# Kernel optimization log

Hardware: AMD Instinct MI355X
Metric: run time of the kernel (lower is better)

Reference implementation:

```python
import jax, jax.numpy as jnp
import numpy as np

B, S, E, H, SN, LMAX = 128, 512, 768, 16, 100, 5
DH = E // H  # 48

def setup_inputs() -> dict:
    key = jax.random.key(0)
    ks = jax.random.split(key, 10)
    idx = jax.random.randint(ks[0], (B, LMAX), 0, S)
    lengths = jax.random.randint(ks[1], (B,), 1, LMAX + 1)
    valid = jnp.arange(LMAX)[None, :] < lengths[:, None]
    locations = jnp.where(valid, idx, -1)
    return {
        "last_hidden_state": jax.random.normal(ks[2], (B, S, E), jnp.float32),
        "sense_emb": jax.random.normal(ks[3], (B, SN, E), jnp.float32),
        "locations": locations,
        "in_proj_weight": jax.random.normal(ks[4], (3 * E, E), jnp.float32) * 0.02,
        "in_proj_bias": jax.random.normal(ks[5], (3 * E,), jnp.float32) * 0.02,
        "out_proj_weight": jax.random.normal(ks[6], (E, E), jnp.float32) * 0.02,
        "out_proj_bias": jax.random.normal(ks[7], (E,), jnp.float32) * 0.02,
        "linear_weight": jax.random.normal(ks[8], (SN, E), jnp.float32) * 0.02,
        "linear_bias": jax.random.normal(ks[9], (SN,), jnp.float32) * 0.02,
    }

def reference(last_hidden_state, sense_emb, locations, in_proj_weight, in_proj_bias,
              out_proj_weight, out_proj_bias, linear_weight, linear_bias):
    # Ragged gather + mean over the valid (non -1) token locations per row.
    mask = (locations != -1)                                   # [B, LMAX]
    safe = jnp.where(mask, locations, 0)                       # [B, LMAX]
    gathered = jnp.take_along_axis(last_hidden_state, safe[..., None], axis=1)  # [B,LMAX,E]
    cnt = mask.sum(axis=1, keepdims=True).astype(last_hidden_state.dtype)
    pun = (gathered * mask[..., None]).sum(axis=1) / cnt       # [B, E]

    # qkv: prepend pun-word embedding to the sense embeddings -> [B, SN+1, E]
    qkv = jnp.concatenate([pun[:, None, :], sense_emb], axis=1)

    # nn.MultiheadAttention with batch_first=False: axis0 = seq (L=B), axis1 = batch (N=SN+1).
    proj = qkv @ in_proj_weight.T + in_proj_bias               # [L, N, 3E]
    q, k, v = jnp.split(proj, 3, axis=-1)
    L, N = qkv.shape[0], qkv.shape[1]
    q = q.reshape(L, N, H, DH) * (DH ** -0.5)
    k = k.reshape(L, N, H, DH)
    v = v.reshape(L, N, H, DH)
    scores = jnp.einsum('lnhd,mnhd->nhlm', q, k)               # [N,H,L,L]
    attn = jax.nn.softmax(scores, axis=-1)
    ctx = jnp.einsum('nhlm,mnhd->lnhd', attn, v).reshape(L, N, E)
    attn_out = ctx @ out_proj_weight.T + out_proj_bias         # [L, N, E]

    res = attn_out[:, 0, :]                                    # [B, E] (batch slot 0)
    res = res @ linear_weight.T + linear_bias                  # [B, SN]
    return res
```

## Files before the change

### kernel.cpp

```cpp
#include <hip/hip_runtime.h>

#define SEQ 512
#define EMB 768
#define K3E 2304
#define DHD 48

__global__ __launch_bounds__(256) void k0_pun(
    const float* __restrict__ lhs, const int* __restrict__ loc,
    float* __restrict__ pun)
{
  int id = blockIdx.x * 256 + threadIdx.x;
  int row = id / 192;
  int ch  = id - row * 192;
  int cnt = 0;
  float4 s = make_float4(0.f, 0.f, 0.f, 0.f);
#pragma unroll
  for (int j = 0; j < 5; j++) {
    int v = loc[row * 5 + j];
    if (v >= 0) {
      float4 wv = *(const float4*)&lhs[((size_t)row * SEQ + v) * EMB + ch * 4];
      s.x += wv.x; s.y += wv.y; s.z += wv.z; s.w += wv.w;
      cnt++;
    }
  }
  float inv = 1.0f / (float)cnt;
  *(float4*)&pun[(size_t)row * EMB + ch * 4] =
      make_float4(s.x * inv, s.y * inv, s.z * inv, s.w * inv);
}

__global__ __launch_bounds__(512, 4) void k1_gemm_wcomb(
    const float* __restrict__ pun, const float* __restrict__ Bw,
    const float* __restrict__ bias, float* __restrict__ C,
    const float* __restrict__ wlin, const float* __restrict__ wout,
    float* __restrict__ wcomb)
{
  __shared__ float lds[14336];
  const int t = threadIdx.x;
  const int w = t >> 6, l = t & 63;
  const int tx = l & 7, ty = l >> 3;
  const int gm = l & 15, gq = l >> 4;
  const int kbase = w * 96;
  const int AW = w * 1792, BW = AW + 640;

  float4 aF, bF0, bF1;
  float acc[2][4] = {};

#define STAGE_A(b) {                                                         \
    int Ab = AW + (b) * 320;                                                 \
    lds[Ab + (gq*4+0)*20 + gm] = aF.x;                                       \
    lds[Ab + (gq*4+1)*20 + gm] = aF.y;                                       \
    lds[Ab + (gq*4+2)*20 + gm] = aF.z;                                       \
    lds[Ab + (gq*4+3)*20 + gm] = aF.w; }

#define INNER(b) {                                                           \
    int Ab = AW + (b) * 320, Bb = BW + (b) * 576;                            \
    _Pragma("unroll")                                                        \
    for (int kk = 0; kk < 16; kk++) {                                        \
      float2 a  = *(float2*)&lds[Ab + kk * 20 + ty * 2];                     \
      float4 bb = *(float4*)&lds[Bb + kk * 36 + tx * 4];                     \
      acc[0][0] += a.x*bb.x; acc[0][1] += a.x*bb.y;                          \
      acc[0][2] += a.x*bb.z; acc[0][3] += a.x*bb.w;                          \
      acc[1][0] += a.y*bb.x; acc[1][1] += a.y*bb.y;                          \
      acc[1][2] += a.y*bb.z; acc[1][3] += a.y*bb.w;                          \
    } }

  if (blockIdx.x < 576) {
    const int c  = blockIdx.x;
    const int bm = (c / 72) * 16, bn = (c % 72) * 32;
    const int bl = l & 31, bh = l >> 5;
    const float* arow = pun + (size_t)(bm + gm) * EMB;
    const float* brow = Bw + (size_t)(bn + bl) * EMB;

#define G_LOAD(s) {                                                          \
    int k0 = kbase + (s) * 16;                                               \
    aF  = *(const float4*)&arow[k0 + gq * 4];                                \
    bF0 = *(const float4*)&brow[k0 + bh * 8 + 0];                            \
    bF1 = *(const float4*)&brow[k0 + bh * 8 + 4]; }

#define G_WRITE(b) {                                                         \
    STAGE_A(b)                                                               \
    int Bb = BW + (b) * 576;                                                 \
    lds[Bb + (bh*8+0)*36 + bl] = bF0.x; lds[Bb + (bh*8+1)*36 + bl] = bF0.y;  \
    lds[Bb + (bh*8+2)*36 + bl] = bF0.z; lds[Bb + (bh*8+3)*36 + bl] = bF0.w;  \
    lds[Bb + (bh*8+4)*36 + bl] = bF1.x; lds[Bb + (bh*8+5)*36 + bl] = bF1.y;  \
    lds[Bb + (bh*8+6)*36 + bl] = bF1.z; lds[Bb + (bh*8+7)*36 + bl] = bF1.w; }

    G_LOAD(0); G_WRITE(0);
    for (int s = 0; s < 6; s++) {
      int b = s & 1;
      if (s < 5) G_LOAD(s + 1);
      INNER(b);
      if (s < 5) G_WRITE(b ^ 1);
    }
#undef G_LOAD
#undef G_WRITE

#pragma unroll
    for (int i = 0; i < 2; i++)
      *(float4*)&lds[AW + (ty*2 + i) * 32 + tx * 4] =
          make_float4(acc[i][0], acc[i][1], acc[i][2], acc[i][3]);
    __syncthreads();
    int m = t >> 5, n = t & 31;
    float v = lds[0*1792 + t] + lds[1*1792 + t] + lds[2*1792 + t] + lds[3*1792 + t]
            + lds[4*1792 + t] + lds[5*1792 + t] + lds[6*1792 + t] + lds[7*1792 + t]
            + bias[bn + n];
    C[(size_t)(bm + m) * K3E + bn + n] = v;
  } else {
    const int cc = blockIdx.x - 576;
    const int bm = (cc / 24) * 16, bn = (cc % 24) * 32;
    const int wi = l >> 2;
    const int j4 = (l & 3) * 8;
    int arow_i = bm + gm; if (arow_i > 99) arow_i = 99;
    const float* arow = wlin + (size_t)arow_i * EMB;

#define W_LOAD(s) {                                                          \
    int k0 = kbase + (s) * 16;                                               \
    aF  = *(const float4*)&arow[k0 + gq * 4];                                \
    const float* wr = wout + (size_t)(k0 + wi) * EMB + bn + j4;              \
    bF0 = *(const float4*)&wr[0];                                            \
    bF1 = *(const float4*)&wr[4]; }

#define W_WRITE(b) {                                                         \
    STAGE_A(b)                                                               \
    int Bb = BW + (b) * 576;                                                 \
    *(float4*)&lds[Bb + wi*36 + j4]     = bF0;                               \
    *(float4*)&lds[Bb + wi*36 + j4 + 4] = bF1; }

    W_LOAD(0); W_WRITE(0);
    for (int s = 0; s < 6; s++) {
      int b = s & 1;
      if (s < 5) W_LOAD(s + 1);
      INNER(b);
      if (s < 5) W_WRITE(b ^ 1);
    }
#undef W_LOAD
#undef W_WRITE

#pragma unroll
    for (int i = 0; i < 2; i++)
      *(float4*)&lds[AW + (ty*2 + i) * 32 + tx * 4] =
          make_float4(acc[i][0], acc[i][1], acc[i][2], acc[i][3]);
    __syncthreads();
    int m = t >> 5, n = t & 31;
    if (bm + m < 100) {
      float v = lds[0*1792 + t] + lds[1*1792 + t] + lds[2*1792 + t] + lds[3*1792 + t]
              + lds[4*1792 + t] + lds[5*1792 + t] + lds[6*1792 + t] + lds[7*1792 + t];
      wcomb[(size_t)(bm + m) * EMB + bn + n] = v;
    }
  }
#undef STAGE_A
#undef INNER
}

__global__ __launch_bounds__(256) void k2_attn(
    const float* __restrict__ proj, float* __restrict__ ctx)
{
  __shared__ float ks[128][52];
  __shared__ float vs[128][52];
  int h  = blockIdx.x >> 3;
  int l0 = (blockIdx.x & 7) * 16;
  int t  = threadIdx.x;

  for (int i = t; i < 128 * 12; i += 256) {
    int m  = i / 12;
    int dd = (i - m * 12) * 4;
    float4 kv = *(const float4*)&proj[(size_t)m * K3E + EMB     + h * DHD + dd];
    float4 vv = *(const float4*)&proj[(size_t)m * K3E + 2 * EMB + h * DHD + dd];
    *(float4*)&ks[m][dd] = kv;
    *(float4*)&vs[m][dd] = vv;
  }

  int l  = t >> 4;
  int g  = t & 15;
  int lg = l0 + l;
  const float scale = 0.14433756729740643f;
  float q[48];
#pragma unroll
  for (int jj = 0; jj < 12; jj++) {
    float4 qv = *(const float4*)&proj[(size_t)lg * K3E + h * DHD + jj * 4];
    q[jj*4+0] = qv.x * scale; q[jj*4+1] = qv.y * scale;
    q[jj*4+2] = qv.z * scale; q[jj*4+3] = qv.w * scale;
  }
  __syncthreads();

  float sv[8];
  float smax = -1e30f;
#pragma unroll
  for (int jm = 0; jm < 8; jm++) {
    int m = g + jm * 16;
    float s = 0.0f;
#pragma unroll
    for (int dq = 0; dq < 12; dq++) {
      float4 kv = *(const float4*)&ks[m][dq * 4];
      s += q[dq*4+0]*kv.x + q[dq*4+1]*kv.y + q[dq*4+2]*kv.z + q[dq*4+3]*kv.w;
    }
    sv[jm] = s;
    smax = fmaxf(smax, s);
  }
#pragma unroll
  for (int off = 1; off < 16; off <<= 1) smax = fmaxf(smax, __shfl_xor(smax, off));
  float ssum = 0.0f;
#pragma unroll
  for (int jm = 0; jm < 8; jm++) { float e = __expf(sv[jm] - smax); sv[jm] = e; ssum += e; }
#pragma unroll
  for (int off = 1; off < 16; off <<= 1) ssum += __shfl_xor(ssum, off);
  float inv = 1.0f / ssum;
#pragma unroll
  for (int jm = 0; jm < 8; jm++) sv[jm] *= inv;

  float acc[48] = {};
#pragma unroll
  for (int jm = 0; jm < 8; jm++) {
    int m = g + jm * 16;
    float p = sv[jm];
#pragma unroll
    for (int dq = 0; dq < 12; dq++) {
      float4 vv = *(const float4*)&vs[m][dq * 4];
      acc[dq*4+0] += p*vv.x; acc[dq*4+1] += p*vv.y;
      acc[dq*4+2] += p*vv.z; acc[dq*4+3] += p*vv.w;
    }
  }

  {
    float buf[24];
    if (g & 8) {
#pragma unroll
      for (int d = 0; d < 24; d++) buf[d] = acc[d];
    } else {
#pragma unroll
      for (int d = 0; d < 24; d++) buf[d] = acc[d + 24];
    }
#pragma unroll
    for (int d = 0; d < 24; d++) buf[d] = __shfl_xor(buf[d], 8);
    if (g & 8) {
#pragma unroll
      for (int d = 0; d < 24; d++) acc[d] = acc[d + 24] + buf[d];
    } else {
#pragma unroll
      for (int d = 0; d < 24; d++) acc[d] = acc[d] + buf[d];
    }
  }
  {
    float buf[12];
    if (g & 4) {
#pragma unroll
      for (int d = 0; d < 12; d++) buf[d] = acc[d];
    } else {
#pragma unroll
      for (int d = 0; d < 12; d++) buf[d] = acc[d + 12];
    }
#pragma unroll
    for (int d = 0; d < 12; d++) buf[d] = __shfl_xor(buf[d], 4);
    if (g & 4) {
#pragma unroll
      for (int d = 0; d < 12; d++) acc[d] = acc[d + 12] + buf[d];
    } else {
#pragma unroll
      for (int d = 0; d < 12; d++) acc[d] = acc[d] + buf[d];
    }
  }
  {
    float buf[6];
    if (g & 2) {
#pragma unroll
      for (int d = 0; d < 6; d++) buf[d] = acc[d];
    } else {
#pragma unroll
      for (int d = 0; d < 6; d++) buf[d] = acc[d + 6];
    }
#pragma unroll
    for (int d = 0; d < 6; d++) buf[d] = __shfl_xor(buf[d], 2);
    if (g & 2) {
#pragma unroll
      for (int d = 0; d < 6; d++) acc[d] = acc[d + 6] + buf[d];
    } else {
#pragma unroll
      for (int d = 0; d < 6; d++) acc[d] = acc[d] + buf[d];
    }
  }
  {
    float buf[3];
    if (g & 1) {
#pragma unroll
      for (int d = 0; d < 3; d++) buf[d] = acc[d];
    } else {
#pragma unroll
      for (int d = 0; d < 3; d++) buf[d] = acc[d + 3];
    }
#pragma unroll
    for (int d = 0; d < 3; d++) buf[d] = __shfl_xor(buf[d], 1);
    if (g & 1) {
#pragma unroll
      for (int d = 0; d < 3; d++) acc[d] = acc[d + 3] + buf[d];
    } else {
#pragma unroll
      for (int d = 0; d < 3; d++) acc[d] = acc[d] + buf[d];
    }
  }
#pragma unroll
  for (int j = 0; j < 3; j++) {
    ctx[(size_t)lg * EMB + h * DHD + g * 3 + j] = acc[j];
  }
}

__global__ __launch_bounds__(512, 4) void k3_final(
    const float* __restrict__ A, const float* __restrict__ Bw,
    const float* __restrict__ wlin, const float* __restrict__ bout,
    const float* __restrict__ blin, float* __restrict__ C)
{
  __shared__ float lds[14368];
  const int t = threadIdx.x;
  const int w = t >> 6, l = t & 63;
  const int bm = blockIdx.y * 16, bn = blockIdx.x * 32;
  const int tx = l & 7, ty = l >> 3;
  const int gm = l & 15, gq = l >> 4;
  const int bl = l & 31, bh = l >> 5;
  const int kbase = w * 96;
  const int AW = w * 1792, BW = AW + 640;

  if (t < 256) {
    int col = bn + (t >> 3);
    int ks  = (t & 7) * 96;
    float p = 0.f;
    if (col < 100) {
      const float* wr = wlin + (size_t)col * EMB + ks;
#pragma unroll
      for (int j = 0; j < 24; j++) {
        float4 wv = *(const float4*)&wr[j * 4];
        float4 bv = *(const float4*)&bout[ks + j * 4];
        p += wv.x*bv.x + wv.y*bv.y + wv.z*bv.z + wv.w*bv.w;
      }
    }
    p += __shfl_xor(p, 1); p += __shfl_xor(p, 2); p += __shfl_xor(p, 4);
    if ((t & 7) == 0) lds[14336 + (t >> 3)] = p + (col < 100 ? blin[col] : 0.f);
  }

  const float* arow = A + (size_t)(bm + gm) * EMB;
  int brow_i = bn + bl; if (brow_i > 99) brow_i = 99;
  const float* brow = Bw + (size_t)brow_i * EMB;

  float4 aF, bF0, bF1;

#define F_LOAD(s) {                                                          \
    int k0 = kbase + (s) * 16;                                               \
    aF  = *(const float4*)&arow[k0 + gq * 4];                                \
    bF0 = *(const float4*)&brow[k0 + bh * 8 + 0];                            \
    bF1 = *(const float4*)&brow[k0 + bh * 8 + 4]; }

#define F_WRITE(b) {                                                         \
    int Ab = AW + (b) * 320;                                                 \
    lds[Ab + (gq*4+0)*20 + gm] = aF.x;                                       \
    lds[Ab + (gq*4+1)*20 + gm] = aF.y;                                       \
    lds[Ab + (gq*4+2)*20 + gm] = aF.z;                                       \
    lds[Ab + (gq*4+3)*20 + gm] = aF.w;                                       \
    int Bb = BW + (b) * 576;                                                 \
    lds[Bb + (bh*8+0)*36 + bl] = bF0.x; lds[Bb + (bh*8+1)*36 + bl] = bF0.y;  \
    lds[Bb + (bh*8+2)*36 + bl] = bF0.z; lds[Bb + (bh*8+3)*36 + bl] = bF0.w;  \
    lds[Bb + (bh*8+4)*36 + bl] = bF1.x; lds[Bb + (bh*8+5)*36 + bl] = bF1.y;  \
    lds[Bb + (bh*8+6)*36 + bl] = bF1.z; lds[Bb + (bh*8+7)*36 + bl] = bF1.w; }

  float acc[2][4] = {};
  F_LOAD(0); F_WRITE(0);
  for (int s = 0; s < 6; s++) {
    int b = s & 1;
    if (s < 5) F_LOAD(s + 1);
    int Ab = AW + b * 320, Bb = BW + b * 576;
#pragma unroll
    for (int kk = 0; kk < 16; kk++) {
      float2 a  = *(float2*)&lds[Ab + kk * 20 + ty * 2];
      float4 bb = *(float4*)&lds[Bb + kk * 36 + tx * 4];
      acc[0][0] += a.x*bb.x; acc[0][1] += a.x*bb.y; acc[0][2] += a.x*bb.z; acc[0][3] += a.x*bb.w;
      acc[1][0] += a.y*bb.x; acc[1][1] += a.y*bb.y; acc[1][2] += a.y*bb.z; acc[1][3] += a.y*bb.w;
    }
    if (s < 5) F_WRITE(b ^ 1);
  }
#undef F_LOAD
#undef F_WRITE

#pragma unroll
  for (int i = 0; i < 2; i++)
    *(float4*)&lds[AW + (ty*2 + i) * 32 + tx * 4] =
        make_float4(acc[i][0], acc[i][1], acc[i][2], acc[i][3]);
  __syncthreads();
  int m = t >> 5, n = t & 31;
  int col = bn + n;
  if (col < 100) {
    float v = lds[0*1792 + t] + lds[1*1792 + t] + lds[2*1792 + t] + lds[3*1792 + t]
            + lds[4*1792 + t] + lds[5*1792 + t] + lds[6*1792 + t] + lds[7*1792 + t]
            + lds[14336 + n];
    C[(size_t)(bm + m) * 100 + col] = v;
  }
}

extern "C" void kernel_launch(void* const* d_in, const int* in_sizes, int n_in,
                              void* d_out, int out_size, void* d_ws, size_t ws_size,
                              hipStream_t stream) {
  const float* lhs   = (const float*)d_in[0];
  const int*   loc   = (const int*)  d_in[2];
  const float* w_in  = (const float*)d_in[3];
  const float* b_in  = (const float*)d_in[4];
  const float* w_out = (const float*)d_in[5];
  const float* b_out = (const float*)d_in[6];
  const float* w_lin = (const float*)d_in[7];
  const float* b_lin = (const float*)d_in[8];
  float* out = (float*)d_out;

  char* ws = (char*)d_ws;
  float* pun   = (float*)(ws);
  float* proj  = (float*)(ws + 393216);
  float* ctx   = (float*)(ws + 393216 + 1179648);
  float* wcomb = (float*)(ws + 393216 + 1179648 + 393216);

  k0_pun<<<96, 256, 0, stream>>>(lhs, loc, pun);
  k1_gemm_wcomb<<<744, 512, 0, stream>>>(pun, w_in, b_in, proj,
                                         w_lin, w_out, wcomb);
  k2_attn<<<128, 256, 0, stream>>>(proj, ctx);
  k3_final<<<dim3(4, 8), 512, 0, stream>>>(ctx, wcomb, w_lin, b_out, b_lin, out);
}
```

Baseline: 45.93 us.

## Widen k1 GEMM tiles to 16x64 and hoist bias dot-product into k1

The k1 GEMM tile grows from 16x32 to 16x64 per block, with each thread holding a 4x4 accumulator and a k-step of 8. This halves the block count from 744 to 372 and raises arithmetic per LDS load. The wlin·bout bias vector is now computed once by an extra block in k1 and written to workspace, instead of being recomputed inside every k3 block. The cost is fewer blocks in flight to hide latency, and k3 now reads the bias from global memory.

```diff
diff --git a/kernel.cpp b/kernel.cpp
--- a/kernel.cpp
+++ b/kernel.cpp
@@ -32,124 +32,160 @@
     const float* __restrict__ pun, const float* __restrict__ Bw,
     const float* __restrict__ bias, float* __restrict__ C,
     const float* __restrict__ wlin, const float* __restrict__ wout,
-    float* __restrict__ wcomb)
+    const float* __restrict__ bout, const float* __restrict__ blin,
+    float* __restrict__ wcomb, float* __restrict__ wsbias)
 {
-  __shared__ float lds[14336];
+  __shared__ float lds[11264];
   const int t = threadIdx.x;
   const int w = t >> 6, l = t & 63;
-  const int tx = l & 7, ty = l >> 3;
-  const int gm = l & 15, gq = l >> 4;
+  const int tx = l & 15, ty = l >> 4;
+  const int gm = l & 15, gk = l >> 4;
   const int kbase = w * 96;
-  const int AW = w * 1792, BW = AW + 640;
-
-  float4 aF, bF0, bF1;
-  float acc[2][4] = {};
-
-#define STAGE_A(b) {                                                         \
-    int Ab = AW + (b) * 320;                                                 \
-    lds[Ab + (gq*4+0)*20 + gm] = aF.x;                                       \
-    lds[Ab + (gq*4+1)*20 + gm] = aF.y;                                       \
-    lds[Ab + (gq*4+2)*20 + gm] = aF.z;                                       \
-    lds[Ab + (gq*4+3)*20 + gm] = aF.w; }
+  const int AW = w * 1408, BW = AW + 320;
+
+  float2 aF;
+  float4 bF0, bF1;
+  float acc[4][4] = {};
+
+#define A_WRITE(b) {                                                         \
+    int Ab = AW + (b) * 160;                                                 \
+    lds[Ab + (gk*2+0)*20 + gm] = aF.x;                                       \
+    lds[Ab + (gk*2+1)*20 + gm] = aF.y; }
 
 #define INNER(b) {                                                           \
-    int Ab = AW + (b) * 320, Bb = BW + (b) * 576;                            \
+    int Ab = AW + (b) * 160, Bb = BW + (b) * 544;                            \
     _Pragma("unroll")                                                        \
-    for (int kk = 0; kk < 16; kk++) {                                        \
-      float2 a  = *(float2*)&lds[Ab + kk * 20 + ty * 2];                     \
-      float4 bb = *(float4*)&lds[Bb + kk * 36 + tx * 4];                     \
+    for (int kk = 0; kk < 8; kk++) {                                         \
+      float4 a  = *(float4*)&lds[Ab + kk * 20 + ty * 4];                     \
+      float4 bb = *(float4*)&lds[Bb + kk * 68 + tx * 4];                     \
       acc[0][0] += a.x*bb.x; acc[0][1] += a.x*bb.y;                          \
       acc[0][2] += a.x*bb.z; acc[0][3] += a.x*bb.w;                          \
       acc[1][0] += a.y*bb.x; acc[1][1] += a.y*bb.y;                          \
       acc[1][2] += a.y*bb.z; acc[1][3] += a.y*bb.w;                          \
+      acc[2][0] += a.z*bb.x; acc[2][1] += a.z*bb.y;                          \
+      acc[2][2] += a.z*bb.z; acc[2][3] += a.z*bb.w;                          \
+      acc[3][0] += a.w*bb.x; acc[3][1] += a.w*bb.y;                          \
+      acc[3][2] += a.w*bb.z; acc[3][3] += a.w*bb.w;                          \
     } }
 
-  if (blockIdx.x < 576) {
+#define EPILOGUE_STORE() {                                                   \
+    _Pragma("unroll")                                                        \
+    for (int i = 0; i < 4; i++)                                              \
+      *(float4*)&lds[AW + (ty*4 + i) * 64 + tx * 4] =                        \
+          make_float4(acc[i][0], acc[i][1], acc[i][2], acc[i][3]);           \
+    __syncthreads(); }
+
+  if (blockIdx.x < 288) {
     const int c  = blockIdx.x;
-    const int bm = (c / 72) * 16, bn = (c % 72) * 32;
-    const int bl = l & 31, bh = l >> 5;
+    const int bm = (c / 36) * 16, bn = (c % 36) * 64;
     const float* arow = pun + (size_t)(bm + gm) * EMB;
-    const float* brow = Bw + (size_t)(bn + bl) * EMB;
+    const float* brow = Bw + (size_t)(bn + l) * EMB;
 
 #define G_LOAD(s) {                                                          \
-    int k0 = kbase + (s) * 16;                                               \
-    aF  = *(const float4*)&arow[k0 + gq * 4];                                \
-    bF0 = *(const float4*)&brow[k0 + bh * 8 + 0];                            \
-    bF1 = *(const float4*)&brow[k0 + bh * 8 + 4]; }
+    int k0 = kbase + (s) * 8;                                                \
+    aF  = *(const float2*)&arow[k0 + gk * 2];                                \
+    bF0 = *(const float4*)&brow[k0 + 0];                                     \
+    bF1 = *(const float4*)&brow[k0 + 4]; }
 
 #define G_WRITE(b) {                                                         \
-    STAGE_A(b)                                                               \
-    int Bb = BW + (b) * 576;                                                 \
-    lds[Bb + (bh*8+0)*36 + bl] = bF0.x; lds[Bb + (bh*8+1)*36 + bl] = bF0.y;  \
-    lds[Bb + (bh*8+2)*36 + bl] = bF0.z; lds[Bb + (bh*8+3)*36 + bl] = bF0.w;  \
-    lds[Bb + (bh*8+4)*36 + bl] = bF1.x; lds[Bb + (bh*8+5)*36 + bl] = bF1.y;  \
-    lds[Bb + (bh*8+6)*36 + bl] = bF1.z; lds[Bb + (bh*8+7)*36 + bl] = bF1.w; }
+    A_WRITE(b)                                                               \
+    int Bb = BW + (b) * 544;                                                 \
+    lds[Bb + 0*68 + l] = bF0.x; lds[Bb + 1*68 + l] = bF0.y;                  \
+    lds[Bb + 2*68 + l] = bF0.z; lds[Bb + 3*68 + l] = bF0.w;                  \
+    lds[Bb + 4*68 + l] = bF1.x; lds[Bb + 5*68 + l] = bF1.y;                  \
+    lds[Bb + 6*68 + l] = bF1.z; lds[Bb + 7*68 + l] = bF1.w; }
 
     G_LOAD(0); G_WRITE(0);
-    for (int s = 0; s < 6; s++) {
+    for (int s = 0; s < 12; s++) {
       int b = s & 1;
-      if (s < 5) G_LOAD(s + 1);
+      if (s < 11) G_LOAD(s + 1);
       INNER(b);
-      if (s < 5) G_WRITE(b ^ 1);
+      if (s < 11) G_WRITE(b ^ 1);
     }
 #undef G_LOAD
 #undef G_WRITE
 
-#pragma unroll
-    for (int i = 0; i < 2; i++)
-      *(float4*)&lds[AW + (ty*2 + i) * 32 + tx * 4] =
-          make_float4(acc[i][0], acc[i][1], acc[i][2], acc[i][3]);
-    __syncthreads();
-    int m = t >> 5, n = t & 31;
-    float v = lds[0*1792 + t] + lds[1*1792 + t] + lds[2*1792 + t] + lds[3*1792 + t]
-            + lds[4*1792 + t] + lds[5*1792 + t] + lds[6*1792 + t] + lds[7*1792 + t]
-            + bias[bn + n];
-    C[(size_t)(bm + m) * K3E + bn + n] = v;
-  } else {
-    const int cc = blockIdx.x - 576;
-    const int bm = (cc / 24) * 16, bn = (cc % 24) * 32;
-    const int wi = l >> 2;
-    const int j4 = (l & 3) * 8;
+    EPILOGUE_STORE();
+    int o = t * 2;
+    int m = o >> 6, n = o & 63;
+    float2 s0 = *(float2*)&lds[0*1408 + o];
+    float2 s1 = *(float2*)&lds[1*1408 + o];
+    float2 s2 = *(float2*)&lds[2*1408 + o];
+    float2 s3 = *(float2*)&lds[3*1408 + o];
+    float2 s4 = *(float2*)&lds[4*1408 + o];
+    float2 s5 = *(float2*)&lds[5*1408 + o];
+    float2 s6 = *(float2*)&lds[6*1408 + o];
+    float2 s7 = *(float2*)&lds[7*1408 + o];
+    float2 bb2 = *(const float2*)&bias[bn + n];
+    float2 r = make_float2(s0.x+s1.x+s2.x+s3.x+s4.x+s5.x+s6.x+s7.x+bb2.x,
+                           s0.y+s1.y+s2.y+s3.y+s4.y+s5.y+s6.y+s7.y+bb2.y);
+    *(float2*)&C[(size_t)(bm + m) * K3E + bn + n] = r;
+  } else if (blockIdx.x < 372) {
+    const int cc = blockIdx.x - 288;
+    const int bm = (cc / 12) * 16, bn = (cc % 12) * 64;
+    const int kr = l >> 3;
+    const int j8 = (l & 7) * 8;
     int arow_i = bm + gm; if (arow_i > 99) arow_i = 99;
     const float* arow = wlin + (size_t)arow_i * EMB;
 
 #define W_LOAD(s) {                                                          \
-    int k0 = kbase + (s) * 16;                                               \
-    aF  = *(const float4*)&arow[k0 + gq * 4];                                \
-    const float* wr = wout + (size_t)(k0 + wi) * EMB + bn + j4;              \
+    int k0 = kbase + (s) * 8;                                                \
+    aF = *(const float2*)&arow[k0 + gk * 2];                                 \
+    const float* wr = wout + (size_t)(k0 + kr) * EMB + bn + j8;              \
     bF0 = *(const float4*)&wr[0];                                            \
     bF1 = *(const float4*)&wr[4]; }
 
 #define W_WRITE(b) {                                                         \
-    STAGE_A(b)                                                               \
-    int Bb = BW + (b) * 576;                                                 \
-    *(float4*)&lds[Bb + wi*36 + j4]     = bF0;                               \
-    *(float4*)&lds[Bb + wi*36 + j4 + 4] = bF1; }
+    A_WRITE(b)                                                               \
+    int Bb = BW + (b) * 544;                                                 \
+    *(float4*)&lds[Bb + kr*68 + j8]     = bF0;                               \
+    *(float4*)&lds[Bb + kr*68 + j8 + 4] = bF1; }
 
     W_LOAD(0); W_WRITE(0);
-    for (int s = 0; s < 6; s++) {
+    for (int s = 0; s < 12; s++) {
       int b = s & 1;
-      if (s < 5) W_LOAD(s + 1);
+      if (s < 11) W_LOAD(s + 1);
       INNER(b);
-      if (s < 5) W_WRITE(b ^ 1);
+      if (s < 11) W_WRITE(b ^ 1);
     }
 #undef W_LOAD
 #undef W_WRITE
 
-#pragma unroll
-    for (int i = 0; i < 2; i++)
-      *(float4*)&lds[AW + (ty*2 + i) * 32 + tx * 4] =
-          make_float4(acc[i][0], acc[i][1], acc[i][2], acc[i][3]);
-    __syncthreads();
-    int m = t >> 5, n = t & 31;
+    EPILOGUE_STORE();
+    int o = t * 2;
+    int m = o >> 6, n = o & 63;
     if (bm + m < 100) {
-      float v = lds[0*1792 + t] + lds[1*1792 + t] + lds[2*1792 + t] + lds[3*1792 + t]
-              + lds[4*1792 + t] + lds[5*1792 + t] + lds[6*1792 + t] + lds[7*1792 + t];
-      wcomb[(size_t)(bm + m) * EMB + bn + n] = v;
-    }
-  }
-#undef STAGE_A
+      float2 s0 = *(float2*)&lds[0*1408 + o];
+      float2 s1 = *(float2*)&lds[1*1408 + o];
+      float2 s2 = *(float2*)&lds[2*1408 + o];
+      float2 s3 = *(float2*)&lds[3*1408 + o];
+      float2 s4 = *(float2*)&lds[4*1408 + o];
+      float2 s5 = *(float2*)&lds[5*1408 + o];
+      float2 s6 = *(float2*)&lds[6*1408 + o];
+      float2 s7 = *(float2*)&lds[7*1408 + o];
+      float2 r = make_float2(s0.x+s1.x+s2.x+s3.x+s4.x+s5.x+s6.x+s7.x,
+                             s0.y+s1.y+s2.y+s3.y+s4.y+s5.y+s6.y+s7.y);
+      *(float2*)&wcomb[(size_t)(bm + m) * EMB + bn + n] = r;
+    }
+  } else {
+    if (t < 400) {
+      int col = t >> 2, q = t & 3;
+      const float* wr = wlin + (size_t)col * EMB + q * 192;
+      const float* br = bout + q * 192;
+      float p = 0.f;
+#pragma unroll
+      for (int j = 0; j < 48; j++) {
+        float4 wv = *(const float4*)&wr[j * 4];
+        float4 bv = *(const float4*)&br[j * 4];
+        p += wv.x*bv.x + wv.y*bv.y + wv.z*bv.z + wv.w*bv.w;
+      }
+      p += __shfl_xor(p, 1); p += __shfl_xor(p, 2);
+      if (q == 0) wsbias[col] = p + blin[col];
+    }
+  }
+#undef A_WRITE
 #undef INNER
+#undef EPILOGUE_STORE
 }
 
 __global__ __launch_bounds__(256) void k2_attn(
@@ -305,10 +341,9 @@
 
 __global__ __launch_bounds__(512, 4) void k3_final(
     const float* __restrict__ A, const float* __restrict__ Bw,
-    const float* __restrict__ wlin, const float* __restrict__ bout,
-    const float* __restrict__ blin, float* __restrict__ C)
+    const float* __restrict__ wsbias, float* __restrict__ C)
 {
-  __shared__ float lds[14368];
+  __shared__ float lds[14336];
   const int t = threadIdx.x;
   const int w = t >> 6, l = t & 63;
   const int bm = blockIdx.y * 16, bn = blockIdx.x * 32;
@@ -317,23 +352,6 @@
   const int bl = l & 31, bh = l >> 5;
   const int kbase = w * 96;
   const int AW = w * 1792, BW = AW + 640;
-
-  if (t < 256) {
-    int col = bn + (t >> 3);
-    int ks  = (t & 7) * 96;
-    float p = 0.f;
-    if (col < 100) {
-      const float* wr = wlin + (size_t)col * EMB + ks;
-#pragma unroll
-      for (int j = 0; j < 24; j++) {
-        float4 wv = *(const float4*)&wr[j * 4];
-        float4 bv = *(const float4*)&bout[ks + j * 4];
-        p += wv.x*bv.x + wv.y*bv.y + wv.z*bv.z + wv.w*bv.w;
-      }
-    }
-    p += __shfl_xor(p, 1); p += __shfl_xor(p, 2); p += __shfl_xor(p, 4);
-    if ((t & 7) == 0) lds[14336 + (t >> 3)] = p + (col < 100 ? blin[col] : 0.f);
-  }
 
   const float* arow = A + (size_t)(bm + gm) * EMB;
   int brow_i = bn + bl; if (brow_i > 99) brow_i = 99;
@@ -387,7 +405,7 @@
   if (col < 100) {
     float v = lds[0*1792 + t] + lds[1*1792 + t] + lds[2*1792 + t] + lds[3*1792 + t]
             + lds[4*1792 + t] + lds[5*1792 + t] + lds[6*1792 + t] + lds[7*1792 + t]
-            + lds[14336 + n];
+            + wsbias[col];
     C[(size_t)(bm + m) * 100 + col] = v;
   }
 }
@@ -406,14 +424,16 @@
   float* out = (float*)d_out;
 
   char* ws = (char*)d_ws;
-  float* pun   = (float*)(ws);
-  float* proj  = (float*)(ws + 393216);
-  float* ctx   = (float*)(ws + 393216 + 1179648);
-  float* wcomb = (float*)(ws + 393216 + 1179648 + 393216);
+  float* pun    = (float*)(ws);
+  float* proj   = (float*)(ws + 393216);
+  float* ctx    = (float*)(ws + 1572864);
+  float* wcomb  = (float*)(ws + 1966080);
+  float* wsbias = (float*)(ws + 2273280);
 
   k0_pun<<<96, 256, 0, stream>>>(lhs, loc, pun);
-  k1_gemm_wcomb<<<744, 512, 0, stream>>>(pun, w_in, b_in, proj,
-                                         w_lin, w_out, wcomb);
+  k1_gemm_wcomb<<<373, 512, 0, stream>>>(pun, w_in, b_in, proj,
+                                         w_lin, w_out, b_out, b_lin,
+                                         wcomb, wsbias);
   k2_attn<<<128, 256, 0, stream>>>(proj, ctx);
-  k3_final<<<dim3(4, 8), 512, 0, stream>>>(ctx, wcomb, w_lin, b_out, b_lin, out);
+  k3_final<<<dim3(4, 8), 512, 0, stream>>>(ctx, wcomb, wsbias, out);
 }
```

Result: slower. 52.05 us (+13.3%).

## Fuse final projection into attention kernel via per-head atomic accumulation

Applied to the files above, without the earlier changes.

Drops the separate final GEMM kernel. Each attention block now stages its 16x48 context tile in shared memory and multiplies it by the matching 48-column slice of the combined weight, adding partial results into the output with atomics. The output is zeroed in the pun kernel, and the bias term (b_out projected through w_lin, plus b_lin) is computed by one extra block of the first GEMM kernel. This removes a kernel launch and the context round trip through global memory, at the cost of 16-way atomic contention per output element and a nondeterministic summation order.

```diff
diff --git a/kernel.cpp b/kernel.cpp
--- a/kernel.cpp
+++ b/kernel.cpp
@@ -7,9 +7,11 @@
 
 __global__ __launch_bounds__(256) void k0_pun(
     const float* __restrict__ lhs, const int* __restrict__ loc,
-    float* __restrict__ pun)
+    float* __restrict__ pun, float* __restrict__ outz)
 {
   int id = blockIdx.x * 256 + threadIdx.x;
+  if (id < 3200)
+    *(float4*)&outz[id * 4] = make_float4(0.f, 0.f, 0.f, 0.f);
   int row = id / 192;
   int ch  = id - row * 192;
   int cnt = 0;
@@ -32,13 +34,15 @@
     const float* __restrict__ pun, const float* __restrict__ Bw,
     const float* __restrict__ bias, float* __restrict__ C,
     const float* __restrict__ wlin, const float* __restrict__ wout,
-    float* __restrict__ wcomb)
+    const float* __restrict__ bout, const float* __restrict__ blin,
+    float* __restrict__ wcomb, float* __restrict__ wsbias)
 {
   __shared__ float lds[14336];
   const int t = threadIdx.x;
   const int w = t >> 6, l = t & 63;
   const int tx = l & 7, ty = l >> 3;
   const int gm = l & 15, gq = l >> 4;
+  const int bl = l & 31, bh = l >> 5;
   const int kbase = w * 96;
   const int AW = w * 1792, BW = AW + 640;
 
@@ -67,7 +71,6 @@
   if (blockIdx.x < 576) {
     const int c  = blockIdx.x;
     const int bm = (c / 72) * 16, bn = (c % 72) * 32;
-    const int bl = l & 31, bh = l >> 5;
     const float* arow = pun + (size_t)(bm + gm) * EMB;
     const float* brow = Bw + (size_t)(bn + bl) * EMB;
 
@@ -94,7 +97,6 @@
     }
 #undef G_LOAD
 #undef G_WRITE
-
 #pragma unroll
     for (int i = 0; i < 2; i++)
       *(float4*)&lds[AW + (ty*2 + i) * 32 + tx * 4] =
@@ -105,7 +107,7 @@
             + lds[4*1792 + t] + lds[5*1792 + t] + lds[6*1792 + t] + lds[7*1792 + t]
             + bias[bn + n];
     C[(size_t)(bm + m) * K3E + bn + n] = v;
-  } else {
+  } else if (blockIdx.x < 744) {
     const int cc = blockIdx.x - 576;
     const int bm = (cc / 24) * 16, bn = (cc % 24) * 32;
     const int wi = l >> 2;
@@ -135,7 +137,6 @@
     }
 #undef W_LOAD
 #undef W_WRITE
-
 #pragma unroll
     for (int i = 0; i < 2; i++)
       *(float4*)&lds[AW + (ty*2 + i) * 32 + tx * 4] =
@@ -147,16 +148,34 @@
               + lds[4*1792 + t] + lds[5*1792 + t] + lds[6*1792 + t] + lds[7*1792 + t];
       wcomb[(size_t)(bm + m) * EMB + bn + n] = v;
     }
+  } else {
+    if (t < 400) {
+      int col = t >> 2, q = t & 3;
+      const float* wr = wlin + (size_t)col * EMB + q * 192;
+      const float* br = bout + q * 192;
+      float p = 0.f;
+#pragma unroll
+      for (int j = 0; j < 48; j++) {
+        float4 wv = *(const float4*)&wr[j * 4];
+        float4 bv = *(const float4*)&br[j * 4];
+        p += wv.x*bv.x + wv.y*bv.y + wv.z*bv.z + wv.w*bv.w;
+      }
+      p += __shfl_xor(p, 1); p += __shfl_xor(p, 2);
+      if (q == 0) wsbias[col] = p + blin[col];
+    }
   }
 #undef STAGE_A
 #undef INNER
 }
 
-__global__ __launch_bounds__(256) void k2_attn(
-    const float* __restrict__ proj, float* __restrict__ ctx)
+__global__ __launch_bounds__(256) void k2_attn_fused(
+    const float* __restrict__ proj, const float* __restrict__ wcomb,
+    const float* __restrict__ wsbias, float* __restrict__ out)
 {
-  __shared__ float ks[128][52];
-  __shared__ float vs[128][52];
+  __shared__ float lds[14080];
+  float* ks   = lds;
+  float* vs   = lds + 6656;
+  float* sctx = lds + 13312;
   int h  = blockIdx.x >> 3;
   int l0 = (blockIdx.x & 7) * 16;
   int t  = threadIdx.x;
@@ -166,8 +185,8 @@
     int dd = (i - m * 12) * 4;
     float4 kv = *(const float4*)&proj[(size_t)m * K3E + EMB     + h * DHD + dd];
     float4 vv = *(const float4*)&proj[(size_t)m * K3E + 2 * EMB + h * DHD + dd];
-    *(float4*)&ks[m][dd] = kv;
-    *(float4*)&vs[m][dd] = vv;
+    *(float4*)&ks[m * 52 + dd] = kv;
+    *(float4*)&vs[m * 52 + dd] = vv;
   }
 
   int l  = t >> 4;
@@ -191,7 +210,7 @@
     float s = 0.0f;
 #pragma unroll
     for (int dq = 0; dq < 12; dq++) {
-      float4 kv = *(const float4*)&ks[m][dq * 4];
+      float4 kv = *(const float4*)&ks[m * 52 + dq * 4];
       s += q[dq*4+0]*kv.x + q[dq*4+1]*kv.y + q[dq*4+2]*kv.z + q[dq*4+3]*kv.w;
     }
     sv[jm] = s;
@@ -215,7 +234,7 @@
     float p = sv[jm];
 #pragma unroll
     for (int dq = 0; dq < 12; dq++) {
-      float4 vv = *(const float4*)&vs[m][dq * 4];
+      float4 vv = *(const float4*)&vs[m * 52 + dq * 4];
       acc[dq*4+0] += p*vv.x; acc[dq*4+1] += p*vv.y;
       acc[dq*4+2] += p*vv.z; acc[dq*4+3] += p*vv.w;
     }
@@ -298,97 +317,30 @@
     }
   }
 #pragma unroll
-  for (int j = 0; j < 3; j++) {
-    ctx[(size_t)lg * EMB + h * DHD + g * 3 + j] = acc[j];
-  }
-}
-
-__global__ __launch_bounds__(512, 4) void k3_final(
-    const float* __restrict__ A, const float* __restrict__ Bw,
-    const float* __restrict__ wlin, const float* __restrict__ bout,
-    const float* __restrict__ blin, float* __restrict__ C)
-{
-  __shared__ float lds[14368];
-  const int t = threadIdx.x;
-  const int w = t >> 6, l = t & 63;
-  const int bm = blockIdx.y * 16, bn = blockIdx.x * 32;
-  const int tx = l & 7, ty = l >> 3;
-  const int gm = l & 15, gq = l >> 4;
-  const int bl = l & 31, bh = l >> 5;
-  const int kbase = w * 96;
-  const int AW = w * 1792, BW = AW + 640;
-
-  if (t < 256) {
-    int col = bn + (t >> 3);
-    int ks  = (t & 7) * 96;
-    float p = 0.f;
-    if (col < 100) {
-      const float* wr = wlin + (size_t)col * EMB + ks;
-#pragma unroll
-      for (int j = 0; j < 24; j++) {
-        float4 wv = *(const float4*)&wr[j * 4];
-        float4 bv = *(const float4*)&bout[ks + j * 4];
-        p += wv.x*bv.x + wv.y*bv.y + wv.z*bv.z + wv.w*bv.w;
+  for (int j = 0; j < 3; j++) sctx[l * 48 + g * 3 + j] = acc[j];
+  __syncthreads();
+
+  {
+    int r  = t >> 4;
+    int cg = t & 15;
+    float cr[48];
+#pragma unroll
+    for (int e = 0; e < 48; e++) cr[e] = sctx[r * 48 + e];
+#pragma unroll
+    for (int j = 0; j < 7; j++) {
+      int col = cg * 7 + j;
+      if (col < 100) {
+        const float* wr = wcomb + (size_t)col * EMB + h * DHD;
+        float s = 0.f;
+#pragma unroll
+        for (int e4 = 0; e4 < 12; e4++) {
+          float4 wv = *(const float4*)&wr[e4 * 4];
+          s += cr[e4*4+0]*wv.x + cr[e4*4+1]*wv.y + cr[e4*4+2]*wv.z + cr[e4*4+3]*wv.w;
+        }
+        if (h == 0) s += wsbias[col];
+        atomicAdd(&out[(size_t)(l0 + r) * 100 + col], s);
       }
     }
-    p += __shfl_xor(p, 1); p += __shfl_xor(p, 2); p += __shfl_xor(p, 4);
-    if ((t & 7) == 0) lds[14336 + (t >> 3)] = p + (col < 100 ? blin[col] : 0.f);
-  }
-
-  const float* arow = A + (size_t)(bm + gm) * EMB;
-  int brow_i = bn + bl; if (brow_i > 99) brow_i = 99;
-  const float* brow = Bw + (size_t)brow_i * EMB;
-
-  float4 aF, bF0, bF1;
-
-#define F_LOAD(s) {                                                          \
-    int k0 = kbase + (s) * 16;                                               \
-    aF  = *(const float4*)&arow[k0 + gq * 4];                                \
-    bF0 = *(const float4*)&brow[k0 + bh * 8 + 0];                            \
-    bF1 = *(const float4*)&brow[k0 + bh * 8 + 4]; }
-
-#define F_WRITE(b) {                                                         \
-    int Ab = AW + (b) * 320;                                                 \
-    lds[Ab + (gq*4+0)*20 + gm] = aF.x;                                       \
-    lds[Ab + (gq*4+1)*20 + gm] = aF.y;                                       \
-    lds[Ab + (gq*4+2)*20 + gm] = aF.z;                                       \
-    lds[Ab + (gq*4+3)*20 + gm] = aF.w;                                       \
-    int Bb = BW + (b) * 576;                                                 \
-    lds[Bb + (bh*8+0)*36 + bl] = bF0.x; lds[Bb + (bh*8+1)*36 + bl] = bF0.y;  \
-    lds[Bb + (bh*8+2)*36 + bl] = bF0.z; lds[Bb + (bh*8+3)*36 + bl] = bF0.w;  \
-    lds[Bb + (bh*8+4)*36 + bl] = bF1.x; lds[Bb + (bh*8+5)*36 + bl] = bF1.y;  \
-    lds[Bb + (bh*8+6)*36 + bl] = bF1.z; lds[Bb + (bh*8+7)*36 + bl] = bF1.w; }
-
-  float acc[2][4] = {};
-  F_LOAD(0); F_WRITE(0);
-  for (int s = 0; s < 6; s++) {
-    int b = s & 1;
-    if (s < 5) F_LOAD(s + 1);
-    int Ab = AW + b * 320, Bb = BW + b * 576;
-#pragma unroll
-    for (int kk = 0; kk < 16; kk++) {
-      float2 a  = *(float2*)&lds[Ab + kk * 20 + ty * 2];
-      float4 bb = *(float4*)&lds[Bb + kk * 36 + tx * 4];
-      acc[0][0] += a.x*bb.x; acc[0][1] += a.x*bb.y; acc[0][2] += a.x*bb.z; acc[0][3] += a.x*bb.w;
-      acc[1][0] += a.y*bb.x; acc[1][1] += a.y*bb.y; acc[1][2] += a.y*bb.z; acc[1][3] += a.y*bb.w;
-    }
-    if (s < 5) F_WRITE(b ^ 1);
-  }
-#undef F_LOAD
-#undef F_WRITE
-
-#pragma unroll
-  for (int i = 0; i < 2; i++)
-    *(float4*)&lds[AW + (ty*2 + i) * 32 + tx * 4] =
-        make_float4(acc[i][0], acc[i][1], acc[i][2], acc[i][3]);
-  __syncthreads();
-  int m = t >> 5, n = t & 31;
-  int col = bn + n;
-  if (col < 100) {
-    float v = lds[0*1792 + t] + lds[1*1792 + t] + lds[2*1792 + t] + lds[3*1792 + t]
-            + lds[4*1792 + t] + lds[5*1792 + t] + lds[6*1792 + t] + lds[7*1792 + t]
-            + lds[14336 + n];
-    C[(size_t)(bm + m) * 100 + col] = v;
   }
 }
 
@@ -406,14 +358,14 @@
   float* out = (float*)d_out;
 
   char* ws = (char*)d_ws;
-  float* pun   = (float*)(ws);
-  float* proj  = (float*)(ws + 393216);
-  float* ctx   = (float*)(ws + 393216 + 1179648);
-  float* wcomb = (float*)(ws + 393216 + 1179648 + 393216);
-
-  k0_pun<<<96, 256, 0, stream>>>(lhs, loc, pun);
-  k1_gemm_wcomb<<<744, 512, 0, stream>>>(pun, w_in, b_in, proj,
-                                         w_lin, w_out, wcomb);
-  k2_attn<<<128, 256, 0, stream>>>(proj, ctx);
-  k3_final<<<dim3(4, 8), 512, 0, stream>>>(ctx, wcomb, w_lin, b_out, b_lin, out);
+  float* pun    = (float*)(ws);
+  float* proj   = (float*)(ws + 393216);
+  float* wcomb  = (float*)(ws + 1572864);
+  float* wsbias = (float*)(ws + 1880064);
+
+  k0_pun<<<96, 256, 0, stream>>>(lhs, loc, pun, out);
+  k1_gemm_wcomb<<<745, 512, 0, stream>>>(pun, w_in, b_in, proj,
+                                         w_lin, w_out, b_out, b_lin,
+                                         wcomb, wsbias);
+  k2_attn_fused<<<128, 256, 0, stream>>>(proj, wcomb, wsbias, out);
 }
```

Result: slower. 56.57 us (+23.2%).
